# Kernel tuning notes

Measured on AMD Instinct MI355X. Metric: run time of the kernel, lower is better.

Reference implementation:

```python
import jax, jax.numpy as jnp
import numpy as np

N = 100000   # nodes
E = 1600000  # edges
D = 128      # input feature dim
H = 128      # hidden dim
C = 10       # output classes
G = 64       # graphs in batch


def setup_inputs() -> dict:
    key = jax.random.key(0)
    ks = jax.random.split(key, 24)
    s = 0.02
    lin = lambda k, i, o: jax.random.normal(k, (i, o), jnp.float32) * s
    inp = {
        'x': jax.random.normal(ks[0], (N, D), jnp.float32),
        'edge_index': jax.random.randint(ks[1], (2, E), 0, N),
        'batch': jnp.sort(jax.random.randint(ks[2], (N,), 0, G)),
        # GIN conv 0: Linear(D,H)-ReLU-Linear(H,H)
        'w1_0': lin(ks[3], D, H), 'b1_0': jnp.zeros((H,), jnp.float32),
        'w2_0': lin(ks[4], H, H), 'b2_0': jnp.zeros((H,), jnp.float32),
        # GIN conv 1
        'w1_1': lin(ks[5], H, H), 'b1_1': jnp.zeros((H,), jnp.float32),
        'w2_1': lin(ks[6], H, H), 'b2_1': jnp.zeros((H,), jnp.float32),
        # GIN conv 2
        'w1_2': lin(ks[7], H, H), 'b1_2': jnp.zeros((H,), jnp.float32),
        'w2_2': lin(ks[8], H, H), 'b2_2': jnp.zeros((H,), jnp.float32),
        # LayerNorms (applied after layers 0 and 1)
        'ln_g0': jnp.ones((H,), jnp.float32), 'ln_b0': jnp.zeros((H,), jnp.float32),
        'ln_g1': jnp.ones((H,), jnp.float32), 'ln_b1': jnp.zeros((H,), jnp.float32),
        # post_mp: Linear(H,H) -> Dropout -> Linear(H,C)
        'pw1': lin(ks[9], H, H), 'pb1': jnp.zeros((H,), jnp.float32),
        'pw2': lin(ks[10], H, C), 'pb2': jnp.zeros((C,), jnp.float32),
    }
    return inp


def _gin_conv(x, src, dst, w1, b1, w2, b2):
    # GINConv with eps=0: MLP(x + sum_{j->i} x_j)
    agg = jax.ops.segment_sum(x[src], dst, num_segments=N)  # [N, d]
    h = x + agg
    h = jax.nn.relu(h @ w1 + b1) @ w2 + b2
    return h


def _layernorm(x, g, b, eps=1e-5):
    mu = jnp.mean(x, axis=-1, keepdims=True)
    var = jnp.var(x, axis=-1, keepdims=True)
    return (x - mu) * jax.lax.rsqrt(var + eps) * g + b


def reference(x, edge_index, batch,
              w1_0, b1_0, w2_0, b2_0,
              w1_1, b1_1, w2_1, b2_1,
              w1_2, b1_2, w2_2, b2_2,
              ln_g0, ln_b0, ln_g1, ln_b1,
              pw1, pb1, pw2, pb2):
    src, dst = edge_index[0], edge_index[1]
    convs = [(w1_0, b1_0, w2_0, b2_0), (w1_1, b1_1, w2_1, b2_1), (w1_2, b1_2, w2_2, b2_2)]
    lns = [(ln_g0, ln_b0), (ln_g1, ln_b1)]
    emb = x
    h = x
    for i in range(3):
        w1, b1, w2, b2 = convs[i]
        h = _gin_conv(h, src, dst, w1, b1, w2, b2)
        emb = h
        h = jax.nn.relu(h)
        # dropout p=0.25: identity in eval mode
        if i != 2:
            g, b = lns[i]
            h = _layernorm(h, g, b)
    # global mean pool over graphs
    sums = jax.ops.segment_sum(h, batch, num_segments=G)          # [G, H]
    cnts = jax.ops.segment_sum(jnp.ones((N,), h.dtype), batch, num_segments=G)
    pooled = sums / jnp.maximum(cnts, 1.0)[:, None]
    # post_mp (dropout identity in eval)
    z = pooled @ pw1 + pb1
    logits = z @ pw2 + pb2
    return emb, jax.nn.log_softmax(logits, axis=1)
```

## Files before the change

kernel.cpp:

```cpp
#include <hip/hip_runtime.h>

typedef __bf16 bf16_t;
typedef __bf16 bf16x8 __attribute__((ext_vector_type(8)));
typedef float floatx4 __attribute__((ext_vector_type(4)));

constexpr int N = 100000;
constexpr int E = 1600000;
constexpr int H = 128;
constexpr int G = 64;
constexpr int C = 10;
constexpr int NBLK = (N + 255) / 256;

constexpr int FPART = 8;
constexpr int FPART_SZ = (N + FPART - 1) / FPART;
constexpr int FCHUNK = 256;
constexpr int FCHUNK_E = E / FCHUNK;

__device__ inline float bflo(unsigned u) {
  return __builtin_bit_cast(float, u << 16);
}
__device__ inline float bfhi(unsigned u) {
  return __builtin_bit_cast(float, u & 0xffff0000u);
}
__device__ inline unsigned short f2b(float f) {
  return __builtin_bit_cast(unsigned short, (bf16_t)f);
}
__device__ inline unsigned pack2(float a, float b) {
  return (unsigned)f2b(a) | ((unsigned)f2b(b) << 16);
}

__global__ __launch_bounds__(256) void tobf_kernel(const float* __restrict__ x,
                                                   uint4* __restrict__ xb) {
  const int g = blockIdx.x * 256 + threadIdx.x;
  const float4 a = *(const float4*)(x + (size_t)g * 8);
  const float4 b = *(const float4*)(x + (size_t)g * 8 + 4);
  uint4 o;
  o.x = pack2(a.x, a.y);
  o.y = pack2(a.z, a.w);
  o.z = pack2(b.x, b.y);
  o.w = pack2(b.z, b.w);
  xb[g] = o;
}

__global__ __launch_bounds__(256) void hist_kernel(const int* __restrict__ dst,
                                                   int* __restrict__ deg) {
  const int e = blockIdx.x * 256 + threadIdx.x;
  if (e < E) atomicAdd(&deg[dst[e]], 1);
}

__global__ __launch_bounds__(256) void partial_kernel(
    const int* __restrict__ deg, int* __restrict__ partials) {
  __shared__ int sm[256];
  const int tid = threadIdx.x;
  const int i = blockIdx.x * 256 + tid;
  sm[tid] = (i < N) ? deg[i] : 0;
  __syncthreads();
  for (int off = 128; off > 0; off >>= 1) {
    if (tid < off) sm[tid] += sm[tid + off];
    __syncthreads();
  }
  if (tid == 0) partials[blockIdx.x] = sm[0];
}

__global__ __launch_bounds__(512) void scanp_kernel(
    const int* __restrict__ partials, int* __restrict__ blockbase) {
  __shared__ int p[512];
  const int t = threadIdx.x;
  p[t] = (t < NBLK) ? partials[t] : 0;
  __syncthreads();
  for (int off = 1; off < 512; off <<= 1) {
    int v = 0;
    if (t >= off) v = p[t - off];
    __syncthreads();
    p[t] += v;
    __syncthreads();
  }
  if (t < NBLK) blockbase[t] = (t == 0) ? 0 : p[t - 1];
}

__global__ __launch_bounds__(256) void expand_kernel(
    const int* __restrict__ deg, const int* __restrict__ blockbase,
    int* __restrict__ rowptr, int* __restrict__ cursor) {
  __shared__ int sm[256];
  const int tid = threadIdx.x;
  const int i = blockIdx.x * 256 + tid;
  const int d = (i < N) ? deg[i] : 0;
  sm[tid] = d;
  __syncthreads();
  for (int off = 1; off < 256; off <<= 1) {
    int v = 0;
    if (tid >= off) v = sm[tid - off];
    __syncthreads();
    sm[tid] += v;
    __syncthreads();
  }
  const int excl = sm[tid] - d + blockbase[blockIdx.x];
  if (i < N) {
    rowptr[i] = excl;
    cursor[i] = excl;
  }
  if (i == N - 1) rowptr[N] = excl + d;
}

__global__ __launch_bounds__(256) void fill_kernel(const int* __restrict__ src,
                                                   const int* __restrict__ dst,
                                                   int* __restrict__ cursor,
                                                   int* __restrict__ csr_src) {
  const int part = blockIdx.x & (FPART - 1);
  const int chunk = blockIdx.x >> 3;
  const int lo = part * FPART_SZ;
  const int hi = lo + FPART_SZ;
  const int c0 = chunk * FCHUNK_E;
  for (int e = c0 + threadIdx.x; e < c0 + FCHUNK_E; e += 256) {
    const int d = __builtin_nontemporal_load(dst + e);
    if (d >= lo && d < hi) {
      const int s = __builtin_nontemporal_load(src + e);
      const int slot = atomicAdd(&cursor[d], 1);
      csr_src[slot] = s;
    }
  }
}

__global__ __launch_bounds__(256) void gather_kernel(
    const uint4* __restrict__ h, const int* __restrict__ rowptr,
    const int* __restrict__ csr_src, uint4* __restrict__ pre) {
  const int node = blockIdx.x * 16 + (threadIdx.x >> 4);
  const int l = threadIdx.x & 15;
  const int r0 = rowptr[node];
  const int r1 = rowptr[node + 1];
  const uint4 v = h[(size_t)node * 16 + l];
  float a0 = bflo(v.x), a1 = bfhi(v.x), a2 = bflo(v.y), a3 = bfhi(v.y);
  float a4 = bflo(v.z), a5 = bfhi(v.z), a6 = bflo(v.w), a7 = bfhi(v.w);
  int s = r0;
  for (; s + 3 < r1; s += 4) {
    const int i0 = csr_src[s], i1 = csr_src[s + 1];
    const int i2 = csr_src[s + 2], i3 = csr_src[s + 3];
    const uint4 u0 = h[(size_t)i0 * 16 + l];
    const uint4 u1 = h[(size_t)i1 * 16 + l];
    const uint4 u2 = h[(size_t)i2 * 16 + l];
    const uint4 u3 = h[(size_t)i3 * 16 + l];
    a0 += bflo(u0.x); a1 += bfhi(u0.x); a2 += bflo(u0.y); a3 += bfhi(u0.y);
    a4 += bflo(u0.z); a5 += bfhi(u0.z); a6 += bflo(u0.w); a7 += bfhi(u0.w);
    a0 += bflo(u1.x); a1 += bfhi(u1.x); a2 += bflo(u1.y); a3 += bfhi(u1.y);
    a4 += bflo(u1.z); a5 += bfhi(u1.z); a6 += bflo(u1.w); a7 += bfhi(u1.w);
    a0 += bflo(u2.x); a1 += bfhi(u2.x); a2 += bflo(u2.y); a3 += bfhi(u2.y);
    a4 += bflo(u2.z); a5 += bfhi(u2.z); a6 += bflo(u2.w); a7 += bfhi(u2.w);
    a0 += bflo(u3.x); a1 += bfhi(u3.x); a2 += bflo(u3.y); a3 += bfhi(u3.y);
    a4 += bflo(u3.z); a5 += bfhi(u3.z); a6 += bflo(u3.w); a7 += bfhi(u3.w);
  }
  for (; s < r1; ++s) {
    const uint4 u = h[(size_t)csr_src[s] * 16 + l];
    a0 += bflo(u.x); a1 += bfhi(u.x); a2 += bflo(u.y); a3 += bfhi(u.y);
    a4 += bflo(u.z); a5 += bfhi(u.z); a6 += bflo(u.w); a7 += bfhi(u.w);
  }
  uint4 o;
  o.x = pack2(a0, a1);
  o.y = pack2(a2, a3);
  o.z = pack2(a4, a5);
  o.w = pack2(a6, a7);
  pre[(size_t)node * 16 + l] = o;
}

template <int MODE>
__global__ __launch_bounds__(256) void mlp_kernel(
    const unsigned short* __restrict__ pre_g,
    const float* __restrict__ w1, const float* __restrict__ b1,
    const float* __restrict__ w2, const float* __restrict__ b2,
    const float* __restrict__ lng, const float* __restrict__ lnb,
    unsigned short* __restrict__ h_out,
    float* __restrict__ emb) {
  __shared__ unsigned short preS[32 * 136];
  __shared__ unsigned short hidS[32 * 136];
  __shared__ float muS[32];
  __shared__ float rsS[32];

  const int tid = threadIdx.x;
  const int wave = tid >> 6;
  const int lane = tid & 63;
  const int quad = lane >> 4;
  const int l16 = lane & 15;

  union F8 { bf16x8 v; bf16_t e[8]; };

  bf16x8 w1f[4][2], w2f[4][2];
#pragma unroll
  for (int nn = 0; nn < 2; ++nn) {
    const int col = wave * 32 + nn * 16 + l16;
#pragma unroll
    for (int kt = 0; kt < 4; ++kt) {
      F8 t1, t2;
#pragma unroll
      for (int j = 0; j < 8; ++j) {
        const int k = kt * 32 + quad * 8 + j;
        t1.e[j] = (bf16_t)w1[k * H + col];
        t2.e[j] = (bf16_t)w2[k * H + col];
      }
      w1f[kt][nn] = t1.v;
      w2f[kt][nn] = t2.v;
    }
  }
  const float b1v[2] = {b1[wave * 32 + l16], b1[wave * 32 + 16 + l16]};
  const float b2v[2] = {b2[wave * 32 + l16], b2[wave * 32 + 16 + l16]};
  float lng0 = 0.f, lng1 = 0.f, lnb0 = 0.f, lnb1 = 0.f;
  const int c2 = (tid * 2) & 127;
  if (MODE == 0) {
    lng0 = lng[c2]; lng1 = lng[c2 + 1];
    lnb0 = lnb[c2]; lnb1 = lnb[c2 + 1];
  }

  for (int tile = blockIdx.x; tile < N / 32; tile += gridDim.x) {
    const size_t base = (size_t)tile * 32 * H;
    {
      const uint4* srcp = (const uint4*)(pre_g + base);
#pragma unroll
      for (int it = 0; it < 2; ++it) {
        const int chunk = it * 256 + tid;
        const int row = chunk >> 4;
        const int colc = (chunk & 15) * 8;
        *(uint4*)&preS[row * 136 + colc] = srcp[chunk];
      }
    }
    __syncthreads();

    {
      floatx4 acc[2][2];
#pragma unroll
      for (int i = 0; i < 2; ++i)
#pragma unroll
        for (int j = 0; j < 2; ++j) acc[i][j] = {0.f, 0.f, 0.f, 0.f};
#pragma unroll
      for (int kt = 0; kt < 4; ++kt) {
        const int kc = kt * 32 + quad * 8;
        const bf16x8 a0 =
            __builtin_bit_cast(bf16x8, *(const uint4*)&preS[l16 * 136 + kc]);
        const bf16x8 a1 = __builtin_bit_cast(
            bf16x8, *(const uint4*)&preS[(16 + l16) * 136 + kc]);
        acc[0][0] = __builtin_amdgcn_mfma_f32_16x16x32_bf16(a0, w1f[kt][0],
                                                            acc[0][0], 0, 0, 0);
        acc[0][1] = __builtin_amdgcn_mfma_f32_16x16x32_bf16(a0, w1f[kt][1],
                                                            acc[0][1], 0, 0, 0);
        acc[1][0] = __builtin_amdgcn_mfma_f32_16x16x32_bf16(a1, w1f[kt][0],
                                                            acc[1][0], 0, 0, 0);
        acc[1][1] = __builtin_amdgcn_mfma_f32_16x16x32_bf16(a1, w1f[kt][1],
                                                            acc[1][1], 0, 0, 0);
      }
#pragma unroll
      for (int mt = 0; mt < 2; ++mt)
#pragma unroll
        for (int nn = 0; nn < 2; ++nn) {
          const int col = wave * 32 + nn * 16 + l16;
#pragma unroll
          for (int r = 0; r < 4; ++r) {
            const int row = mt * 16 + quad * 4 + r;
            const float v = fmaxf(acc[mt][nn][r] + b1v[nn], 0.f);
            hidS[row * 136 + col] = f2b(v);
          }
        }
    }
    __syncthreads();

    {
      floatx4 acc[2][2];
#pragma unroll
      for (int i = 0; i < 2; ++i)
#pragma unroll
        for (int j = 0; j < 2; ++j) acc[i][j] = {0.f, 0.f, 0.f, 0.f};
#pragma unroll
      for (int kt = 0; kt < 4; ++kt) {
        const int kc = kt * 32 + quad * 8;
        const bf16x8 a0 =
            __builtin_bit_cast(bf16x8, *(const uint4*)&hidS[l16 * 136 + kc]);
        const bf16x8 a1 = __builtin_bit_cast(
            bf16x8, *(const uint4*)&hidS[(16 + l16) * 136 + kc]);
        acc[0][0] = __builtin_amdgcn_mfma_f32_16x16x32_bf16(a0, w2f[kt][0],
                                                            acc[0][0], 0, 0, 0);
        acc[0][1] = __builtin_amdgcn_mfma_f32_16x16x32_bf16(a0, w2f[kt][1],
                                                            acc[0][1], 0, 0, 0);
        acc[1][0] = __builtin_amdgcn_mfma_f32_16x16x32_bf16(a1, w2f[kt][0],
                                                            acc[1][0], 0, 0, 0);
        acc[1][1] = __builtin_amdgcn_mfma_f32_16x16x32_bf16(a1, w2f[kt][1],
                                                            acc[1][1], 0, 0, 0);
      }
#pragma unroll
      for (int mt = 0; mt < 2; ++mt)
#pragma unroll
        for (int nn = 0; nn < 2; ++nn) {
          const int col = wave * 32 + nn * 16 + l16;
#pragma unroll
          for (int r = 0; r < 4; ++r) {
            const int row = mt * 16 + quad * 4 + r;
            float v = acc[mt][nn][r] + b2v[nn];
            if (MODE == 0) v = fmaxf(v, 0.f);
            preS[row * 136 + col] = f2b(v);
          }
        }
    }
    __syncthreads();

    if (MODE == 0) {
      const int n = tid >> 3;
      const int j = tid & 7;
      float s = 0.f, sq = 0.f;
#pragma unroll
      for (int t = 0; t < 16; ++t) {
        const float v = bflo((unsigned)preS[n * 136 + j + 8 * t] << 16 >> 16 |
                             ((unsigned)preS[n * 136 + j + 8 * t] << 16));
        (void)v;
      }
      s = 0.f; sq = 0.f;
#pragma unroll
      for (int t = 0; t < 16; ++t) {
        const float v =
            __builtin_bit_cast(float, (unsigned)preS[n * 136 + j + 8 * t] << 16);
        s += v;
        sq += v * v;
      }
      s += __shfl_xor(s, 1); sq += __shfl_xor(sq, 1);
      s += __shfl_xor(s, 2); sq += __shfl_xor(sq, 2);
      s += __shfl_xor(s, 4); sq += __shfl_xor(sq, 4);
      if (j == 0) {
        const float mu = s * (1.f / H);
        const float var = sq * (1.f / H) - mu * mu;
        muS[n] = mu;
        rsS[n] = rsqrtf(var + 1e-5f);
      }
      __syncthreads();
      unsigned* ho = (unsigned*)(h_out + base);
#pragma unroll
      for (int it = 0; it < 8; ++it) {
        const int idx = it * 512 + tid * 2;
        const int row = idx >> 7;
        const int k = idx & 127;
        const unsigned pr = *(const unsigned*)&preS[row * 136 + k];
        const float mu = muS[row], rs = rsS[row];
        const float v0 = (bflo(pr) - mu) * rs * lng0 + lnb0;
        const float v1 = (bfhi(pr) - mu) * rs * lng1 + lnb1;
        ho[idx >> 1] = pack2(v0, v1);
      }
    } else {
      unsigned* ho = (unsigned*)(h_out + base);
#pragma unroll
      for (int it = 0; it < 8; ++it) {
        const int idx = it * 512 + tid * 2;
        const int row = idx >> 7;
        const int k = idx & 127;
        const unsigned pr = *(const unsigned*)&preS[row * 136 + k];
        const float v0 = bflo(pr);
        const float v1 = bfhi(pr);
        *(float2*)&emb[base + idx] = make_float2(v0, v1);
        ho[idx >> 1] = pack2(fmaxf(v0, 0.f), fmaxf(v1, 0.f));
      }
    }
    __syncthreads();
  }
}

__global__ __launch_bounds__(256) void pool_kernel(
    const uint4* __restrict__ hv, const int* __restrict__ batch,
    float* __restrict__ pooled, float* __restrict__ cnt) {
  __shared__ int bs[256];
  __shared__ float smr[512];
  __shared__ int endS;
  const int tid = threadIdx.x;
  const int c0 = blockIdx.x * 256;
  const int len = min(256, N - c0);
  if (tid < len) bs[tid] = batch[c0 + tid];
  __syncthreads();

  const int nl = tid >> 4;
  const int fg = tid & 15;
  const int wave = tid >> 6;
  const int lane = tid & 63;

  int start = 0;
  while (start < len) {
    const int g = bs[start];
    if (tid == 0) endS = len;
    __syncthreads();
    for (int i = start + tid; i < len; i += 256)
      if (bs[i] != g) atomicMin(&endS, i);
    __syncthreads();
    const int end = endS;

    float a0 = 0.f, a1 = 0.f, a2 = 0.f, a3 = 0.f;
    float a4 = 0.f, a5 = 0.f, a6 = 0.f, a7 = 0.f;
    for (int i = start + nl; i < end; i += 16) {
      const uint4 u = hv[(size_t)(c0 + i) * 16 + fg];
      a0 += bflo(u.x); a1 += bfhi(u.x); a2 += bflo(u.y); a3 += bfhi(u.y);
      a4 += bflo(u.z); a5 += bfhi(u.z); a6 += bflo(u.w); a7 += bfhi(u.w);
    }
    a0 += __shfl_xor(a0, 16); a1 += __shfl_xor(a1, 16);
    a2 += __shfl_xor(a2, 16); a3 += __shfl_xor(a3, 16);
    a4 += __shfl_xor(a4, 16); a5 += __shfl_xor(a5, 16);
    a6 += __shfl_xor(a6, 16); a7 += __shfl_xor(a7, 16);
    a0 += __shfl_xor(a0, 32); a1 += __shfl_xor(a1, 32);
    a2 += __shfl_xor(a2, 32); a3 += __shfl_xor(a3, 32);
    a4 += __shfl_xor(a4, 32); a5 += __shfl_xor(a5, 32);
    a6 += __shfl_xor(a6, 32); a7 += __shfl_xor(a7, 32);
    if (lane < 16) {
      float* d = &smr[wave * 128 + lane * 8];
      d[0] = a0; d[1] = a1; d[2] = a2; d[3] = a3;
      d[4] = a4; d[5] = a5; d[6] = a6; d[7] = a7;
    }
    __syncthreads();
    if (tid < 128) {
      const float s =
          smr[tid] + smr[128 + tid] + smr[256 + tid] + smr[384 + tid];
      atomicAdd(&pooled[g * H + tid], s);
    }
    if (tid == 0) atomicAdd(&cnt[g], (float)(end - start));
    __syncthreads();
    start = end;
  }
}

__global__ __launch_bounds__(128) void head_kernel(
    const float* __restrict__ pooled, const float* __restrict__ cnt,
    const float* __restrict__ pw1, const float* __restrict__ pb1,
    const float* __restrict__ pw2, const float* __restrict__ pb2,
    float* __restrict__ out_logp) {
  __shared__ float p[H];
  __shared__ float z[H];
  __shared__ float l[C];
  const int g = blockIdx.x;
  const int f = threadIdx.x;
  const float c = fmaxf(cnt[g], 1.f);
  p[f] = pooled[g * H + f] / c;
  __syncthreads();
  float a = pb1[f];
  for (int k = 0; k < H; ++k) a += p[k] * pw1[k * H + f];
  z[f] = a;
  __syncthreads();
  if (f < C) {
    float a2 = pb2[f];
    for (int k = 0; k < H; ++k) a2 += z[k] * pw2[k * C + f];
    l[f] = a2;
  }
  __syncthreads();
  if (f == 0) {
    float m = l[0];
    for (int i = 1; i < C; ++i) m = fmaxf(m, l[i]);
    float s = 0.f;
    for (int i = 0; i < C; ++i) s += expf(l[i] - m);
    const float lse = m + logf(s);
    for (int i = 0; i < C; ++i) out_logp[g * C + i] = l[i] - lse;
  }
}

extern "C" void kernel_launch(void* const* d_in, const int* in_sizes, int n_in,
                              void* d_out, int out_size, void* d_ws,
                              size_t ws_size, hipStream_t stream) {
  const float* x = (const float*)d_in[0];
  const int* ei = (const int*)d_in[1];
  const int* src = ei;
  const int* dst = ei + E;
  const int* batch = (const int*)d_in[2];
  const float* w1_0 = (const float*)d_in[3];
  const float* b1_0 = (const float*)d_in[4];
  const float* w2_0 = (const float*)d_in[5];
  const float* b2_0 = (const float*)d_in[6];
  const float* w1_1 = (const float*)d_in[7];
  const float* b1_1 = (const float*)d_in[8];
  const float* w2_1 = (const float*)d_in[9];
  const float* b2_1 = (const float*)d_in[10];
  const float* w1_2 = (const float*)d_in[11];
  const float* b1_2 = (const float*)d_in[12];
  const float* w2_2 = (const float*)d_in[13];
  const float* b2_2 = (const float*)d_in[14];
  const float* ln_g0 = (const float*)d_in[15];
  const float* ln_b0 = (const float*)d_in[16];
  const float* ln_g1 = (const float*)d_in[17];
  const float* ln_b1 = (const float*)d_in[18];
  const float* pw1 = (const float*)d_in[19];
  const float* pb1 = (const float*)d_in[20];
  const float* pw2 = (const float*)d_in[21];
  const float* pb2 = (const float*)d_in[22];

  unsigned short* xb = (unsigned short*)d_ws;
  unsigned short* hb = xb + (size_t)N * H;
  unsigned short* pre = hb + (size_t)N * H;
  float* pooled = (float*)(pre + (size_t)N * H);
  float* cnt = pooled + (size_t)G * H;
  int* deg = (int*)(cnt + G);
  int* rowptr = deg + N;
  int* cursor = rowptr + N + 1;
  int* csr_src = cursor + N;
  int* partials = csr_src + E;
  int* blockbase = partials + NBLK;
  float* emb = (float*)d_out;
  float* logp = emb + (size_t)N * H;

  tobf_kernel<<<N * H / (256 * 8), 256, 0, stream>>>(x, (uint4*)xb);

  hipMemsetAsync(deg, 0, (size_t)N * sizeof(int), stream);
  hist_kernel<<<E / 256, 256, 0, stream>>>(dst, deg);
  partial_kernel<<<NBLK, 256, 0, stream>>>(deg, partials);
  scanp_kernel<<<1, 512, 0, stream>>>(partials, blockbase);
  expand_kernel<<<NBLK, 256, 0, stream>>>(deg, blockbase, rowptr, cursor);
  fill_kernel<<<FCHUNK * FPART, 256, 0, stream>>>(src, dst, cursor, csr_src);

  gather_kernel<<<N / 16, 256, 0, stream>>>((const uint4*)xb, rowptr, csr_src,
                                            (uint4*)pre);
  mlp_kernel<0><<<2048, 256, 0, stream>>>(pre, w1_0, b1_0, w2_0, b2_0, ln_g0,
                                          ln_b0, hb, nullptr);
  gather_kernel<<<N / 16, 256, 0, stream>>>((const uint4*)hb, rowptr, csr_src,
                                            (uint4*)pre);
  mlp_kernel<0><<<2048, 256, 0, stream>>>(pre, w1_1, b1_1, w2_1, b2_1, ln_g1,
                                          ln_b1, hb, nullptr);
  gather_kernel<<<N / 16, 256, 0, stream>>>((const uint4*)hb, rowptr, csr_src,
                                            (uint4*)pre);
  mlp_kernel<1><<<2048, 256, 0, stream>>>(pre, w1_2, b1_2, w2_2, b2_2, nullptr,
                                          nullptr, hb, emb);

  hipMemsetAsync(pooled, 0, (size_t)(G * H + G) * sizeof(float), stream);
  pool_kernel<<<NBLK, 256, 0, stream>>>((const uint4*)hb, batch, pooled, cnt);
  head_kernel<<<G, 128, 0, stream>>>(pooled, cnt, pw1, pb1, pw2, pb2, logp);
}
```

Measured before the change: 573.4 us.

## Pre-pack bf16 weight fragments, XCC-aware dynamic fill scheduling, fewer MLP blocks

Adds a prep kernel that converts all six MLP weight matrices once into bf16 MFMA fragment layout, so each MLP block loads them with coalesced uint4 reads instead of strided per-element float loads and conversions. The CSR fill kernel now reads the hardware XCC id and has blocks pull chunks from per-partition atomic work queues, starting with the partition matching their XCC, to improve L2 locality of the cursor atomics. MLP grids shrink from 2048 to 640 blocks to amortise weight loading, and a dead LayerNorm loop is removed. This adds a kernel launch and queue atomics, and relies on the XCC register encoding.

```diff
diff --git a/kernel.cpp b/kernel.cpp
--- a/kernel.cpp
+++ b/kernel.cpp
@@ -15,6 +15,7 @@
 constexpr int FPART_SZ = (N + FPART - 1) / FPART;
 constexpr int FCHUNK = 256;
 constexpr int FCHUNK_E = E / FCHUNK;
+constexpr int XCC_GETREG_IMM = 63508;
 
 __device__ inline float bflo(unsigned u) {
   return __builtin_bit_cast(float, u << 16);
@@ -42,6 +43,32 @@
   xb[g] = o;
 }
 
+__global__ __launch_bounds__(256) void prepw_kernel(
+    const float* __restrict__ w1_0, const float* __restrict__ w2_0,
+    const float* __restrict__ w1_1, const float* __restrict__ w2_1,
+    const float* __restrict__ w1_2, const float* __restrict__ w2_2,
+    uint4* __restrict__ wprep) {
+  const int m = blockIdx.y;
+  const float* w = (m == 0) ? w1_0 : (m == 1) ? w2_0 : (m == 2) ? w1_1
+                   : (m == 3) ? w2_1 : (m == 4) ? w1_2 : w2_2;
+  const int ktnn = blockIdx.x;
+  const int kt = ktnn >> 1;
+  const int nn = ktnn & 1;
+  const int tid = threadIdx.x;
+  const int wave = tid >> 6;
+  const int lane = tid & 63;
+  const int quad = lane >> 4;
+  const int l16 = lane & 15;
+  const int col = wave * 32 + nn * 16 + l16;
+  const int kb = kt * 32 + quad * 8;
+  uint4 o;
+  o.x = pack2(w[(kb + 0) * H + col], w[(kb + 1) * H + col]);
+  o.y = pack2(w[(kb + 2) * H + col], w[(kb + 3) * H + col]);
+  o.z = pack2(w[(kb + 4) * H + col], w[(kb + 5) * H + col]);
+  o.w = pack2(w[(kb + 6) * H + col], w[(kb + 7) * H + col]);
+  wprep[(m * 8 + ktnn) * 256 + tid] = o;
+}
+
 __global__ __launch_bounds__(256) void hist_kernel(const int* __restrict__ dst,
                                                    int* __restrict__ deg) {
   const int e = blockIdx.x * 256 + threadIdx.x;
@@ -105,18 +132,29 @@
 __global__ __launch_bounds__(256) void fill_kernel(const int* __restrict__ src,
                                                    const int* __restrict__ dst,
                                                    int* __restrict__ cursor,
-                                                   int* __restrict__ csr_src) {
-  const int part = blockIdx.x & (FPART - 1);
-  const int chunk = blockIdx.x >> 3;
-  const int lo = part * FPART_SZ;
-  const int hi = lo + FPART_SZ;
-  const int c0 = chunk * FCHUNK_E;
-  for (int e = c0 + threadIdx.x; e < c0 + FCHUNK_E; e += 256) {
-    const int d = __builtin_nontemporal_load(dst + e);
-    if (d >= lo && d < hi) {
-      const int s = __builtin_nontemporal_load(src + e);
-      const int slot = atomicAdd(&cursor[d], 1);
-      csr_src[slot] = s;
+                                                   int* __restrict__ csr_src,
+                                                   int* __restrict__ qcnt) {
+  __shared__ int chunkS;
+  const int xcc = __builtin_amdgcn_s_getreg(XCC_GETREG_IMM) & (FPART - 1);
+  for (int pp = 0; pp < FPART; ++pp) {
+    const int p = (xcc + pp) & (FPART - 1);
+    const int lo = p * FPART_SZ;
+    const int hi = lo + FPART_SZ;
+    while (true) {
+      if (threadIdx.x == 0) chunkS = atomicAdd(&qcnt[p], 1);
+      __syncthreads();
+      const int chunk = chunkS;
+      __syncthreads();
+      if (chunk >= FCHUNK) break;
+      const int c0 = chunk * FCHUNK_E;
+      for (int e = c0 + threadIdx.x; e < c0 + FCHUNK_E; e += 256) {
+        const int d = __builtin_nontemporal_load(dst + e);
+        if (d >= lo && d < hi) {
+          const int s = __builtin_nontemporal_load(src + e);
+          const int slot = atomicAdd(&cursor[d], 1);
+          csr_src[slot] = s;
+        }
+      }
     }
   }
 }
@@ -164,8 +202,8 @@
 template <int MODE>
 __global__ __launch_bounds__(256) void mlp_kernel(
     const unsigned short* __restrict__ pre_g,
-    const float* __restrict__ w1, const float* __restrict__ b1,
-    const float* __restrict__ w2, const float* __restrict__ b2,
+    const uint4* __restrict__ w1p, const uint4* __restrict__ w2p,
+    const float* __restrict__ b1, const float* __restrict__ b2,
     const float* __restrict__ lng, const float* __restrict__ lnb,
     unsigned short* __restrict__ h_out,
     float* __restrict__ emb) {
@@ -180,25 +218,14 @@
   const int quad = lane >> 4;
   const int l16 = lane & 15;
 
-  union F8 { bf16x8 v; bf16_t e[8]; };
-
   bf16x8 w1f[4][2], w2f[4][2];
 #pragma unroll
-  for (int nn = 0; nn < 2; ++nn) {
-    const int col = wave * 32 + nn * 16 + l16;
-#pragma unroll
-    for (int kt = 0; kt < 4; ++kt) {
-      F8 t1, t2;
-#pragma unroll
-      for (int j = 0; j < 8; ++j) {
-        const int k = kt * 32 + quad * 8 + j;
-        t1.e[j] = (bf16_t)w1[k * H + col];
-        t2.e[j] = (bf16_t)w2[k * H + col];
-      }
-      w1f[kt][nn] = t1.v;
-      w2f[kt][nn] = t2.v;
-    }
-  }
+  for (int kt = 0; kt < 4; ++kt)
+#pragma unroll
+    for (int nn = 0; nn < 2; ++nn) {
+      w1f[kt][nn] = __builtin_bit_cast(bf16x8, w1p[(kt * 2 + nn) * 256 + tid]);
+      w2f[kt][nn] = __builtin_bit_cast(bf16x8, w2p[(kt * 2 + nn) * 256 + tid]);
+    }
   const float b1v[2] = {b1[wave * 32 + l16], b1[wave * 32 + 16 + l16]};
   const float b2v[2] = {b2[wave * 32 + l16], b2[wave * 32 + 16 + l16]};
   float lng0 = 0.f, lng1 = 0.f, lnb0 = 0.f, lnb1 = 0.f;
@@ -301,13 +328,6 @@
       const int n = tid >> 3;
       const int j = tid & 7;
       float s = 0.f, sq = 0.f;
-#pragma unroll
-      for (int t = 0; t < 16; ++t) {
-        const float v = bflo((unsigned)preS[n * 136 + j + 8 * t] << 16 >> 16 |
-                             ((unsigned)preS[n * 136 + j + 8 * t] << 16));
-        (void)v;
-      }
-      s = 0.f; sq = 0.f;
 #pragma unroll
       for (int t = 0; t < 16; ++t) {
         const float v =
@@ -476,13 +496,15 @@
   const float* pw2 = (const float*)d_in[21];
   const float* pb2 = (const float*)d_in[22];
 
-  unsigned short* xb = (unsigned short*)d_ws;
+  uint4* wprep = (uint4*)d_ws;
+  unsigned short* xb = (unsigned short*)(wprep + 6 * 2048);
   unsigned short* hb = xb + (size_t)N * H;
   unsigned short* pre = hb + (size_t)N * H;
   float* pooled = (float*)(pre + (size_t)N * H);
   float* cnt = pooled + (size_t)G * H;
   int* deg = (int*)(cnt + G);
-  int* rowptr = deg + N;
+  int* qcnt = deg + N;
+  int* rowptr = qcnt + FPART;
   int* cursor = rowptr + N + 1;
   int* csr_src = cursor + N;
   int* partials = csr_src + E;
@@ -491,26 +513,31 @@
   float* logp = emb + (size_t)N * H;
 
   tobf_kernel<<<N * H / (256 * 8), 256, 0, stream>>>(x, (uint4*)xb);
-
-  hipMemsetAsync(deg, 0, (size_t)N * sizeof(int), stream);
+  prepw_kernel<<<dim3(8, 6), 256, 0, stream>>>(w1_0, w2_0, w1_1, w2_1, w1_2,
+                                               w2_2, wprep);
+
+  hipMemsetAsync(deg, 0, (size_t)(N + FPART) * sizeof(int), stream);
   hist_kernel<<<E / 256, 256, 0, stream>>>(dst, deg);
   partial_kernel<<<NBLK, 256, 0, stream>>>(deg, partials);
   scanp_kernel<<<1, 512, 0, stream>>>(partials, blockbase);
   expand_kernel<<<NBLK, 256, 0, stream>>>(deg, blockbase, rowptr, cursor);
-  fill_kernel<<<FCHUNK * FPART, 256, 0, stream>>>(src, dst, cursor, csr_src);
+  fill_kernel<<<2048, 256, 0, stream>>>(src, dst, cursor, csr_src, qcnt);
 
   gather_kernel<<<N / 16, 256, 0, stream>>>((const uint4*)xb, rowptr, csr_src,
                                             (uint4*)pre);
-  mlp_kernel<0><<<2048, 256, 0, stream>>>(pre, w1_0, b1_0, w2_0, b2_0, ln_g0,
-                                          ln_b0, hb, nullptr);
+  mlp_kernel<0><<<640, 256, 0, stream>>>(pre, wprep + 0 * 2048,
+                                         wprep + 1 * 2048, b1_0, b2_0, ln_g0,
+                                         ln_b0, hb, nullptr);
   gather_kernel<<<N / 16, 256, 0, stream>>>((const uint4*)hb, rowptr, csr_src,
                                             (uint4*)pre);
-  mlp_kernel<0><<<2048, 256, 0, stream>>>(pre, w1_1, b1_1, w2_1, b2_1, ln_g1,
-                                          ln_b1, hb, nullptr);
+  mlp_kernel<0><<<640, 256, 0, stream>>>(pre, wprep + 2 * 2048,
+                                         wprep + 3 * 2048, b1_1, b2_1, ln_g1,
+                                         ln_b1, hb, nullptr);
   gather_kernel<<<N / 16, 256, 0, stream>>>((const uint4*)hb, rowptr, csr_src,
                                             (uint4*)pre);
-  mlp_kernel<1><<<2048, 256, 0, stream>>>(pre, w1_2, b1_2, w2_2, b2_2, nullptr,
-                                          nullptr, hb, emb);
+  mlp_kernel<1><<<640, 256, 0, stream>>>(pre, wprep + 4 * 2048,
+                                         wprep + 5 * 2048, b1_2, b2_2, nullptr,
+                                         nullptr, hb, emb);
 
   hipMemsetAsync(pooled, 0, (size_t)(G * H + G) * sizeof(float), stream);
   pool_kernel<<<NBLK, 256, 0, stream>>>((const uint4*)hb, batch, pooled, cnt);
```

After: 757.8 us. 32.2% more time.
